# Kernel tuning notes

Hardware: AMD Instinct MI355X
Metric: run time of the kernel (lower is better)

The kernel has to match this reference:

```python
import jax, jax.numpy as jnp
import numpy as np

T, B, I, H = 512, 64, 1024, 1024
DROPOUT = 0.3


def setup_inputs() -> dict:
    key = jax.random.key(0)
    k = jax.random.split(key, 6)
    s = 1.0 / np.sqrt(H).astype(np.float32)
    x = jax.random.normal(k[0], (T, B, I), dtype=jnp.float32)
    w_ih = jax.random.uniform(k[1], (4 * H, I), minval=-s, maxval=s, dtype=jnp.float32)
    w_hh = jax.random.uniform(k[2], (4 * H, H), minval=-s, maxval=s, dtype=jnp.float32)
    b_ih = jax.random.uniform(k[3], (4 * H,), minval=-s, maxval=s, dtype=jnp.float32)
    b_hh = jax.random.uniform(k[4], (4 * H,), minval=-s, maxval=s, dtype=jnp.float32)
    # init_weights: forget-gate bias (second quarter) set to 1
    b_ih = b_ih.at[H:2 * H].set(1.0)
    b_hh = b_hh.at[H:2 * H].set(1.0)
    # DropConnect mask on recurrent weights (training-mode dropout, fixed realization)
    keep = jax.random.bernoulli(k[5], 1.0 - DROPOUT, (4 * H, H))
    hh_mask = keep.astype(jnp.float32) / (1.0 - DROPOUT)
    return {"x": x, "w_ih": w_ih, "w_hh": w_hh, "b_ih": b_ih, "b_hh": b_hh, "hh_mask": hh_mask}


def reference(x, w_ih, w_hh, b_ih, b_hh, hh_mask):
    # x: (T, B, I). PyTorch LSTM gate order: i, f, g, o.
    h = w_hh.shape[1]
    w_hh_dropped = w_hh * hh_mask  # DropConnect applied once per forward
    # Precompute input contribution for all timesteps (one big GEMM): (T, B, 4H)
    gx = jnp.einsum('tbi,gi->tbg', x, w_ih) + b_ih + b_hh

    def step(carry, g_t):
        h_t, c_t = carry
        gates = g_t + h_t @ w_hh_dropped.T  # (B, 4H)
        i_g, f_g, g_g, o_g = jnp.split(gates, 4, axis=-1)
        i_g = jax.nn.sigmoid(i_g)
        f_g = jax.nn.sigmoid(f_g)
        g_g = jnp.tanh(g_g)
        o_g = jax.nn.sigmoid(o_g)
        c_new = f_g * c_t + i_g * g_g
        h_new = o_g * jnp.tanh(c_new)
        return (h_new, c_new), h_new

    bsz = x.shape[1]
    init = (jnp.zeros((bsz, h), x.dtype), jnp.zeros((bsz, h), x.dtype))
    (hn, cn), out = jax.lax.scan(step, init, gx)
    # match torch: output (T,B,H), hn/cn with leading num_layers dim
    return out, hn[None], cn[None]
```

## Files before the change

kernel.cpp:

```cpp
#include <hip/hip_runtime.h>

#define TT 512
#define BB 64
#define II 1024
#define HH 1024
#define GG 4096
#define BH 65536
#define NBLK 128

typedef __attribute__((ext_vector_type(8))) short bf16x8;
typedef __attribute__((ext_vector_type(4))) float f32x4;
typedef __attribute__((ext_vector_type(4))) unsigned u32x4;

__device__ __forceinline__ float bf2f(unsigned short u) {
  union { unsigned int i; float f; } v; v.i = ((unsigned int)u) << 16; return v.f;
}
__device__ __forceinline__ unsigned short f2bf(float f) {
  union { float f; unsigned int i; } v; v.f = f;
  return (unsigned short)((v.i + 0x7FFFu + ((v.i >> 16) & 1u)) >> 16);
}
__device__ __forceinline__ bf16x8 pack8(float4 a, float4 b) {
  union { bf16x8 v; unsigned short u[8]; } p;
  p.u[0] = f2bf(a.x); p.u[1] = f2bf(a.y); p.u[2] = f2bf(a.z); p.u[3] = f2bf(a.w);
  p.u[4] = f2bf(b.x); p.u[5] = f2bf(b.y); p.u[6] = f2bf(b.z); p.u[7] = f2bf(b.w);
  return p.v;
}
__device__ __forceinline__ float sigmoid_f(float x) { return 1.0f / (1.0f + __expf(-x)); }
__device__ __forceinline__ float tanh_f(float x) {
  float e = __expf(-2.0f * fabsf(x));
  float t = (1.0f - e) / (1.0f + e);
  return copysignf(t, x);
}

__device__ __forceinline__ void st32_uc(unsigned* p, unsigned v) {
  __hip_atomic_store(p, v, __ATOMIC_RELAXED, __HIP_MEMORY_SCOPE_AGENT);
}
__device__ __forceinline__ unsigned ld32_uc(const unsigned* p) {
  return __hip_atomic_load(p, __ATOMIC_RELAXED, __HIP_MEMORY_SCOPE_AGENT);
}
__device__ __forceinline__ void st128_uc(void* p, u32x4 v) {
  asm volatile("global_store_dwordx4 %0, %1, off sc0 sc1" :: "v"(p), "v"(v) : "memory");
}

__global__ __launch_bounds__(256) void wdlstm_gemm_gx(
    const float* __restrict__ xc, const float* __restrict__ w_ih,
    const float* __restrict__ b_ih, const float* __restrict__ b_hh,
    unsigned short* __restrict__ gxc) {
  __shared__ __align__(16) char As[16384];
  __shared__ __align__(16) char Bs[16384];

  const int tid = threadIdx.x;
  const int bx  = blockIdx.x;
  const int tm  = bx >> 5, tn = bx & 31;
  const int m0  = tm * 128, n0 = tn * 128;
  const int wv  = tid >> 6, l = tid & 63;
  const int wr  = wv >> 1, wc = wv & 1;
  const int ln  = l & 15, lq = l >> 4;

  f32x4 acc[4][4];
#pragma unroll
  for (int i = 0; i < 4; ++i)
#pragma unroll
    for (int j = 0; j < 4; ++j) acc[i][j] = (f32x4){0.f, 0.f, 0.f, 0.f};

  for (int kt = 0; kt < 16; ++kt) {
    const int k0 = kt * 64;
    __syncthreads();
#pragma unroll
    for (int o = 0; o < 4; ++o) {
      int c2 = tid + 256 * o;
      int row = c2 >> 3, q8 = c2 & 7;
      int addr = (row * 128 + q8 * 16) ^ ((row & 7) << 4);
      {
        const float* s = xc + (size_t)(m0 + row) * II + k0 + q8 * 8;
        float4 a0 = *(const float4*)s;
        float4 a1 = *(const float4*)(s + 4);
        *(bf16x8*)(As + addr) = pack8(a0, a1);
      }
      {
        const float* s = w_ih + (size_t)(n0 + row) * II + k0 + q8 * 8;
        float4 a0 = *(const float4*)s;
        float4 a1 = *(const float4*)(s + 4);
        *(bf16x8*)(Bs + addr) = pack8(a0, a1);
      }
    }
    __syncthreads();
#pragma unroll
    for (int kc = 0; kc < 2; ++kc) {
      bf16x8 af[4], bfr[4];
#pragma unroll
      for (int mi = 0; mi < 4; ++mi) {
        int row = 64 * wr + 16 * mi + ln;
        int addr = (row * 128 + kc * 64 + lq * 16) ^ ((row & 7) << 4);
        af[mi] = *(const bf16x8*)(As + addr);
      }
#pragma unroll
      for (int ni = 0; ni < 4; ++ni) {
        int row = 64 * wc + 16 * ni + ln;
        int addr = (row * 128 + kc * 64 + lq * 16) ^ ((row & 7) << 4);
        bfr[ni] = *(const bf16x8*)(Bs + addr);
      }
#pragma unroll
      for (int mi = 0; mi < 4; ++mi)
#pragma unroll
        for (int ni = 0; ni < 4; ++ni)
          acc[mi][ni] = __builtin_amdgcn_mfma_f32_16x16x32_bf16(af[mi], bfr[ni], acc[mi][ni], 0, 0, 0);
    }
  }
#pragma unroll
  for (int mi = 0; mi < 4; ++mi)
#pragma unroll
    for (int ni = 0; ni < 4; ++ni) {
      int col = n0 + 64 * wc + 16 * ni + ln;
      float bv = b_ih[col] + b_hh[col];
#pragma unroll
      for (int r = 0; r < 4; ++r) {
        int row = m0 + 64 * wr + 16 * mi + 4 * lq + r;
        gxc[(size_t)row * GG + col] = f2bf(acc[mi][ni][r] + bv);
      }
    }
}

__global__ __launch_bounds__(256) void wdlstm_recurrence(
    const float* __restrict__ w_hh, const float* __restrict__ hh_mask,
    const unsigned short* __restrict__ gxc,
    float* __restrict__ out, float* __restrict__ c_state,
    unsigned* __restrict__ flags,
    unsigned short* __restrict__ hinit,
    unsigned short* __restrict__ hring,
    int t0, int tc) {
  __shared__ __align__(16) char Wlds[65536];
  __shared__ float Dlds[64][35];
  __shared__ __align__(16) unsigned Hs[64][4];

  const int tid = threadIdx.x;
  const int wv  = tid >> 6, l = tid & 63;
  const int ln  = l & 15, lq = l >> 4;
  const int j0h = blockIdx.x * 8;
  unsigned* g_step = flags + 2048;

#pragma unroll
  for (int c8 = 0; c8 < 16; ++c8) {
    int c = tid + 256 * c8;
    int n = c >> 7, cc = c & 127;
    int wrow = (n >> 3) * HH + j0h + (n & 7);
    const float* sw = w_hh   + (size_t)wrow * HH + cc * 8;
    const float* sm = hh_mask + (size_t)wrow * HH + cc * 8;
    float4 w0 = *(const float4*)sw, w1 = *(const float4*)(sw + 4);
    float4 m0 = *(const float4*)sm, m1 = *(const float4*)(sm + 4);
    float4 p0 = {w0.x * m0.x, w0.y * m0.y, w0.z * m0.z, w0.w * m0.w};
    float4 p1 = {w1.x * m1.x, w1.y * m1.y, w1.z * m1.z, w1.w * m1.w};
    int addr = (n * 2048 + cc * 16) ^ ((n & 7) << 4);
    *(bf16x8*)(Wlds + addr) = pack8(p0, p1);
  }
  __syncthreads();

  const int b_ep = l;
  const int jj0  = 2 * wv;
  float c_reg[2];
  if (t0 == 0) {
    c_reg[0] = c_reg[1] = 0.f;
  } else {
    float2 cv = *(const float2*)(c_state + (size_t)b_ep * HH + j0h + jj0);
    c_reg[0] = cv.x; c_reg[1] = cv.y;
  }

  float* hn_out = out + (size_t)TT * BH;
  float* cn_out = hn_out + BH;

  float gxv[4][2];
#pragma unroll
  for (int g = 0; g < 4; ++g) {
    unsigned u = *(const unsigned*)(gxc + (size_t)b_ep * GG + g * HH + j0h + jj0);
    gxv[g][0] = bf2f((unsigned short)u);
    gxv[g][1] = bf2f((unsigned short)(u >> 16));
  }

  for (int lt = 0; lt < tc; ++lt) {
    const int t = t0 + lt;

    f32x4 acc[2];
    acc[0] = (f32x4){0.f, 0.f, 0.f, 0.f};
    acc[1] = (f32x4){0.f, 0.f, 0.f, 0.f};

    if (t > 0) {
      if (blockIdx.x == 0) {
        if (tid < 64) {
          const unsigned* f0 = flags + (2 * tid) * 16;
          const unsigned* f1 = flags + (2 * tid + 1) * 16;
          while ((int)ld32_uc(f0) < t || (int)ld32_uc(f1) < t)
            __builtin_amdgcn_s_sleep(1);
          if (tid == 0) st32_uc(g_step, (unsigned)t);
        }
        __syncthreads();
      } else {
        if (tid == 0) {
          while ((int)ld32_uc(g_step) < t) __builtin_amdgcn_s_sleep(1);
        }
        __syncthreads();
      }

      const unsigned short* hp = (lt == 0) ? hinit
                                           : hring + (size_t)(lt - 1) * BH;
      const unsigned short* ap = hp + (size_t)(16 * wv + ln) * HH + lq * 8;
#pragma unroll 4
      for (int kc = 0; kc < 32; ++kc) {
        bf16x8 a = *(const bf16x8*)(ap + kc * 32);
#pragma unroll
        for (int ni = 0; ni < 2; ++ni) {
          int n = 16 * ni + ln;
          int baddr = (n * 2048 + kc * 64 + lq * 16) ^ ((n & 7) << 4);
          bf16x8 b = *(const bf16x8*)(Wlds + baddr);
          acc[ni] = __builtin_amdgcn_mfma_f32_16x16x32_bf16(a, b, acc[ni], 0, 0, 0);
        }
      }
    }
#pragma unroll
    for (int ni = 0; ni < 2; ++ni)
#pragma unroll
      for (int r = 0; r < 4; ++r)
        Dlds[16 * wv + 4 * lq + r][16 * ni + ln] = acc[ni][r];
    __syncthreads();

    float hq[2];
#pragma unroll
    for (int q = 0; q < 2; ++q) {
      float g0 = Dlds[b_ep][ 0 + jj0 + q] + gxv[0][q];
      float g1 = Dlds[b_ep][ 8 + jj0 + q] + gxv[1][q];
      float g2 = Dlds[b_ep][16 + jj0 + q] + gxv[2][q];
      float g3 = Dlds[b_ep][24 + jj0 + q] + gxv[3][q];
      float ig = sigmoid_f(g0);
      float fg = sigmoid_f(g1);
      float gg = tanh_f(g2);
      float og = sigmoid_f(g3);
      c_reg[q] = fg * c_reg[q] + ig * gg;
      hq[q] = og * tanh_f(c_reg[q]);
    }
    *(float2*)(out + (size_t)t * BH + (size_t)b_ep * HH + j0h + jj0) = make_float2(hq[0], hq[1]);
    Hs[b_ep][wv] = (unsigned)f2bf(hq[0]) | ((unsigned)f2bf(hq[1]) << 16);
    if (t == TT - 1) {
      *(float2*)(hn_out + (size_t)b_ep * HH + j0h + jj0) = make_float2(hq[0], hq[1]);
      *(float2*)(cn_out + (size_t)b_ep * HH + j0h + jj0) = make_float2(c_reg[0], c_reg[1]);
    }

    if (lt + 1 < tc) {
#pragma unroll
      for (int g = 0; g < 4; ++g) {
        unsigned u = *(const unsigned*)(gxc + ((size_t)(lt + 1) * BB + b_ep) * GG + g * HH + j0h + jj0);
        gxv[g][0] = bf2f((unsigned short)u);
        gxv[g][1] = bf2f((unsigned short)(u >> 16));
      }
    }

    __syncthreads();

    if (wv == 0) {
      u32x4 hv4 = *(const u32x4*)&Hs[l][0];
      char* dst = (char*)hring + ((size_t)lt * BH + (size_t)l * HH + j0h) * 2;
      st128_uc(dst, hv4);
      if (lt == tc - 1) {
        char* dsti = (char*)hinit + ((size_t)l * HH + j0h) * 2;
        st128_uc(dsti, hv4);
      }
      asm volatile("s_waitcnt vmcnt(0)" ::: "memory");
      if (tid == 0) st32_uc(&flags[blockIdx.x * 16], (unsigned)(t + 1));
    }
  }

  *(float2*)(c_state + (size_t)b_ep * HH + j0h + jj0) = make_float2(c_reg[0], c_reg[1]);
}

extern "C" void kernel_launch(void* const* d_in, const int* in_sizes, int n_in,
                              void* d_out, int out_size, void* d_ws, size_t ws_size,
                              hipStream_t stream) {
  const float* x       = (const float*)d_in[0];
  const float* w_ih    = (const float*)d_in[1];
  const float* w_hh    = (const float*)d_in[2];
  const float* b_ih    = (const float*)d_in[3];
  const float* b_hh    = (const float*)d_in[4];
  const float* hh_mask = (const float*)d_in[5];
  float* out           = (float*)d_out;

  char* ws = (char*)d_ws;
  float* c_state        = (float*)ws;
  unsigned* flags       = (unsigned*)(ws + 262144);
  unsigned short* hinit = (unsigned short*)(ws + 278528);
  unsigned short* hring = (unsigned short*)(ws + 409600);

  const long long fixed = 409600;
  const long long per_t = 524288 + 131072;
  long long avail = (long long)ws_size - fixed;
  int TC = (int)(avail / per_t);
  if (TC > 128) TC = 128;
  TC &= ~1;
  if (TC < 2) TC = 2;
  unsigned short* gxc = (unsigned short*)(ws + 409600 + (size_t)TC * 131072);

  hipMemsetAsync(flags, 0, 16384, stream);

  for (int t0 = 0; t0 < TT; t0 += TC) {
    int tc = TT - t0 < TC ? TT - t0 : TC;
    const float* xc = x + (size_t)t0 * BB * II;
    int grid = (tc * 64 / 128) * 32;
    wdlstm_gemm_gx<<<grid, 256, 0, stream>>>(xc, w_ih, b_ih, b_hh, gxc);
    wdlstm_recurrence<<<NBLK, 256, 0, stream>>>(w_hh, hh_mask, gxc, out, c_state,
                                                flags, hinit, hring, t0, tc);
  }
}
```

Before: 4.539 ms.

## Fuse input projection GEMM into persistent recurrence kernel with LDS-resident W_ih slice

Removes the separate big input-projection GEMM and the bf16 gate buffer. Each persistent block now keeps its slice of W_ih in LDS next to W_hh and computes the next timestep's x·W_ih product after publishing h, so that work can fill the wait before the next grid barrier. A small kernel converts x to bf16 beforehand. This doubles LDS use per block to about 128KB and puts 128 blocks' worth of input GEMM onto the serial recurrence path, so it pays off only if that work actually hides behind the barrier latency.

Result: slower. 4.663 ms (+2.7%).

```diff
diff --git a/kernel.cpp b/kernel.cpp
--- a/kernel.cpp
+++ b/kernel.cpp
@@ -42,94 +42,28 @@
   asm volatile("global_store_dwordx4 %0, %1, off sc0 sc1" :: "v"(p), "v"(v) : "memory");
 }
 
-__global__ __launch_bounds__(256) void wdlstm_gemm_gx(
-    const float* __restrict__ xc, const float* __restrict__ w_ih,
+__global__ __launch_bounds__(256) void wdlstm_xconv(
+    const float* __restrict__ xc, unsigned short* __restrict__ xbf, int n4) {
+  int stride = gridDim.x * blockDim.x;
+  for (int i = blockIdx.x * blockDim.x + threadIdx.x; i < n4; i += stride) {
+    float4 v = *(const float4*)(xc + (size_t)i * 4);
+    unsigned short o[4] = {f2bf(v.x), f2bf(v.y), f2bf(v.z), f2bf(v.w)};
+    *(unsigned long long*)(xbf + (size_t)i * 4) = *(unsigned long long*)o;
+  }
+}
+
+__global__ __launch_bounds__(256) void wdlstm_fused(
+    const float* __restrict__ w_hh, const float* __restrict__ hh_mask,
+    const float* __restrict__ w_ih,
     const float* __restrict__ b_ih, const float* __restrict__ b_hh,
-    unsigned short* __restrict__ gxc) {
-  __shared__ __align__(16) char As[16384];
-  __shared__ __align__(16) char Bs[16384];
-
-  const int tid = threadIdx.x;
-  const int bx  = blockIdx.x;
-  const int tm  = bx >> 5, tn = bx & 31;
-  const int m0  = tm * 128, n0 = tn * 128;
-  const int wv  = tid >> 6, l = tid & 63;
-  const int wr  = wv >> 1, wc = wv & 1;
-  const int ln  = l & 15, lq = l >> 4;
-
-  f32x4 acc[4][4];
-#pragma unroll
-  for (int i = 0; i < 4; ++i)
-#pragma unroll
-    for (int j = 0; j < 4; ++j) acc[i][j] = (f32x4){0.f, 0.f, 0.f, 0.f};
-
-  for (int kt = 0; kt < 16; ++kt) {
-    const int k0 = kt * 64;
-    __syncthreads();
-#pragma unroll
-    for (int o = 0; o < 4; ++o) {
-      int c2 = tid + 256 * o;
-      int row = c2 >> 3, q8 = c2 & 7;
-      int addr = (row * 128 + q8 * 16) ^ ((row & 7) << 4);
-      {
-        const float* s = xc + (size_t)(m0 + row) * II + k0 + q8 * 8;
-        float4 a0 = *(const float4*)s;
-        float4 a1 = *(const float4*)(s + 4);
-        *(bf16x8*)(As + addr) = pack8(a0, a1);
-      }
-      {
-        const float* s = w_ih + (size_t)(n0 + row) * II + k0 + q8 * 8;
-        float4 a0 = *(const float4*)s;
-        float4 a1 = *(const float4*)(s + 4);
-        *(bf16x8*)(Bs + addr) = pack8(a0, a1);
-      }
-    }
-    __syncthreads();
-#pragma unroll
-    for (int kc = 0; kc < 2; ++kc) {
-      bf16x8 af[4], bfr[4];
-#pragma unroll
-      for (int mi = 0; mi < 4; ++mi) {
-        int row = 64 * wr + 16 * mi + ln;
-        int addr = (row * 128 + kc * 64 + lq * 16) ^ ((row & 7) << 4);
-        af[mi] = *(const bf16x8*)(As + addr);
-      }
-#pragma unroll
-      for (int ni = 0; ni < 4; ++ni) {
-        int row = 64 * wc + 16 * ni + ln;
-        int addr = (row * 128 + kc * 64 + lq * 16) ^ ((row & 7) << 4);
-        bfr[ni] = *(const bf16x8*)(Bs + addr);
-      }
-#pragma unroll
-      for (int mi = 0; mi < 4; ++mi)
-#pragma unroll
-        for (int ni = 0; ni < 4; ++ni)
-          acc[mi][ni] = __builtin_amdgcn_mfma_f32_16x16x32_bf16(af[mi], bfr[ni], acc[mi][ni], 0, 0, 0);
-    }
-  }
-#pragma unroll
-  for (int mi = 0; mi < 4; ++mi)
-#pragma unroll
-    for (int ni = 0; ni < 4; ++ni) {
-      int col = n0 + 64 * wc + 16 * ni + ln;
-      float bv = b_ih[col] + b_hh[col];
-#pragma unroll
-      for (int r = 0; r < 4; ++r) {
-        int row = m0 + 64 * wr + 16 * mi + 4 * lq + r;
-        gxc[(size_t)row * GG + col] = f2bf(acc[mi][ni][r] + bv);
-      }
-    }
-}
-
-__global__ __launch_bounds__(256) void wdlstm_recurrence(
-    const float* __restrict__ w_hh, const float* __restrict__ hh_mask,
-    const unsigned short* __restrict__ gxc,
+    const unsigned short* __restrict__ xbf,
     float* __restrict__ out, float* __restrict__ c_state,
     unsigned* __restrict__ flags,
     unsigned short* __restrict__ hinit,
     unsigned short* __restrict__ hring,
     int t0, int tc) {
-  __shared__ __align__(16) char Wlds[65536];
+  __shared__ __align__(16) char Wh[65536];
+  __shared__ __align__(16) char Wi[65536];
   __shared__ float Dlds[64][35];
   __shared__ __align__(16) unsigned Hs[64][4];
 
@@ -144,14 +78,21 @@
     int c = tid + 256 * c8;
     int n = c >> 7, cc = c & 127;
     int wrow = (n >> 3) * HH + j0h + (n & 7);
-    const float* sw = w_hh   + (size_t)wrow * HH + cc * 8;
-    const float* sm = hh_mask + (size_t)wrow * HH + cc * 8;
-    float4 w0 = *(const float4*)sw, w1 = *(const float4*)(sw + 4);
-    float4 m0 = *(const float4*)sm, m1 = *(const float4*)(sm + 4);
-    float4 p0 = {w0.x * m0.x, w0.y * m0.y, w0.z * m0.z, w0.w * m0.w};
-    float4 p1 = {w1.x * m1.x, w1.y * m1.y, w1.z * m1.z, w1.w * m1.w};
     int addr = (n * 2048 + cc * 16) ^ ((n & 7) << 4);
-    *(bf16x8*)(Wlds + addr) = pack8(p0, p1);
+    {
+      const float* sw = w_hh   + (size_t)wrow * HH + cc * 8;
+      const float* sm = hh_mask + (size_t)wrow * HH + cc * 8;
+      float4 w0 = *(const float4*)sw, w1 = *(const float4*)(sw + 4);
+      float4 m0 = *(const float4*)sm, m1 = *(const float4*)(sm + 4);
+      float4 p0 = {w0.x * m0.x, w0.y * m0.y, w0.z * m0.z, w0.w * m0.w};
+      float4 p1 = {w1.x * m1.x, w1.y * m1.y, w1.z * m1.z, w1.w * m1.w};
+      *(bf16x8*)(Wh + addr) = pack8(p0, p1);
+    }
+    {
+      const float* si = w_ih + (size_t)wrow * II + cc * 8;
+      float4 a0 = *(const float4*)si, a1 = *(const float4*)(si + 4);
+      *(bf16x8*)(Wi + addr) = pack8(a0, a1);
+    }
   }
   __syncthreads();
 
@@ -164,24 +105,41 @@
     float2 cv = *(const float2*)(c_state + (size_t)b_ep * HH + j0h + jj0);
     c_reg[0] = cv.x; c_reg[1] = cv.y;
   }
+  float biasv[4][2];
+#pragma unroll
+  for (int g = 0; g < 4; ++g)
+#pragma unroll
+    for (int q = 0; q < 2; ++q) {
+      int col = g * HH + j0h + jj0 + q;
+      biasv[g][q] = b_ih[col] + b_hh[col];
+    }
 
   float* hn_out = out + (size_t)TT * BH;
   float* cn_out = hn_out + BH;
 
-  float gxv[4][2];
-#pragma unroll
-  for (int g = 0; g < 4; ++g) {
-    unsigned u = *(const unsigned*)(gxc + (size_t)b_ep * GG + g * HH + j0h + jj0);
-    gxv[g][0] = bf2f((unsigned short)u);
-    gxv[g][1] = bf2f((unsigned short)(u >> 16));
-  }
+  f32x4 gxacc[2];
+  auto gx_compute = [&](int lt) {
+    gxacc[0] = (f32x4){0.f, 0.f, 0.f, 0.f};
+    gxacc[1] = (f32x4){0.f, 0.f, 0.f, 0.f};
+    const unsigned short* ap = xbf + (size_t)lt * BH + (size_t)(16 * wv + ln) * II + lq * 8;
+#pragma unroll 4
+    for (int kc = 0; kc < 32; ++kc) {
+      bf16x8 a = *(const bf16x8*)(ap + kc * 32);
+#pragma unroll
+      for (int ni = 0; ni < 2; ++ni) {
+        int n = 16 * ni + ln;
+        int baddr = (n * 2048 + kc * 64 + lq * 16) ^ ((n & 7) << 4);
+        bf16x8 b = *(const bf16x8*)(Wi + baddr);
+        gxacc[ni] = __builtin_amdgcn_mfma_f32_16x16x32_bf16(a, b, gxacc[ni], 0, 0, 0);
+      }
+    }
+  };
+  gx_compute(0);
 
   for (int lt = 0; lt < tc; ++lt) {
     const int t = t0 + lt;
 
-    f32x4 acc[2];
-    acc[0] = (f32x4){0.f, 0.f, 0.f, 0.f};
-    acc[1] = (f32x4){0.f, 0.f, 0.f, 0.f};
+    f32x4 acc[2] = {gxacc[0], gxacc[1]};
 
     if (t > 0) {
       if (blockIdx.x == 0) {
@@ -210,7 +168,7 @@
         for (int ni = 0; ni < 2; ++ni) {
           int n = 16 * ni + ln;
           int baddr = (n * 2048 + kc * 64 + lq * 16) ^ ((n & 7) << 4);
-          bf16x8 b = *(const bf16x8*)(Wlds + baddr);
+          bf16x8 b = *(const bf16x8*)(Wh + baddr);
           acc[ni] = __builtin_amdgcn_mfma_f32_16x16x32_bf16(a, b, acc[ni], 0, 0, 0);
         }
       }
@@ -225,10 +183,10 @@
     float hq[2];
 #pragma unroll
     for (int q = 0; q < 2; ++q) {
-      float g0 = Dlds[b_ep][ 0 + jj0 + q] + gxv[0][q];
-      float g1 = Dlds[b_ep][ 8 + jj0 + q] + gxv[1][q];
-      float g2 = Dlds[b_ep][16 + jj0 + q] + gxv[2][q];
-      float g3 = Dlds[b_ep][24 + jj0 + q] + gxv[3][q];
+      float g0 = Dlds[b_ep][ 0 + jj0 + q] + biasv[0][q];
+      float g1 = Dlds[b_ep][ 8 + jj0 + q] + biasv[1][q];
+      float g2 = Dlds[b_ep][16 + jj0 + q] + biasv[2][q];
+      float g3 = Dlds[b_ep][24 + jj0 + q] + biasv[3][q];
       float ig = sigmoid_f(g0);
       float fg = sigmoid_f(g1);
       float gg = tanh_f(g2);
@@ -241,15 +199,6 @@
     if (t == TT - 1) {
       *(float2*)(hn_out + (size_t)b_ep * HH + j0h + jj0) = make_float2(hq[0], hq[1]);
       *(float2*)(cn_out + (size_t)b_ep * HH + j0h + jj0) = make_float2(c_reg[0], c_reg[1]);
-    }
-
-    if (lt + 1 < tc) {
-#pragma unroll
-      for (int g = 0; g < 4; ++g) {
-        unsigned u = *(const unsigned*)(gxc + ((size_t)(lt + 1) * BB + b_ep) * GG + g * HH + j0h + jj0);
-        gxv[g][0] = bf2f((unsigned short)u);
-        gxv[g][1] = bf2f((unsigned short)(u >> 16));
-      }
     }
 
     __syncthreads();
@@ -265,6 +214,8 @@
       asm volatile("s_waitcnt vmcnt(0)" ::: "memory");
       if (tid == 0) st32_uc(&flags[blockIdx.x * 16], (unsigned)(t + 1));
     }
+
+    if (lt + 1 < tc) gx_compute(lt + 1);
   }
 
   *(float2*)(c_state + (size_t)b_ep * HH + j0h + jj0) = make_float2(c_reg[0], c_reg[1]);
@@ -288,22 +239,20 @@
   unsigned short* hring = (unsigned short*)(ws + 409600);
 
   const long long fixed = 409600;
-  const long long per_t = 524288 + 131072;
+  const long long per_t = 131072 + 131072;
   long long avail = (long long)ws_size - fixed;
   int TC = (int)(avail / per_t);
   if (TC > 128) TC = 128;
-  TC &= ~1;
   if (TC < 2) TC = 2;
-  unsigned short* gxc = (unsigned short*)(ws + 409600 + (size_t)TC * 131072);
+  unsigned short* xbf = (unsigned short*)(ws + 409600 + (size_t)TC * 131072);
 
   hipMemsetAsync(flags, 0, 16384, stream);
 
   for (int t0 = 0; t0 < TT; t0 += TC) {
     int tc = TT - t0 < TC ? TT - t0 : TC;
     const float* xc = x + (size_t)t0 * BB * II;
-    int grid = (tc * 64 / 128) * 32;
-    wdlstm_gemm_gx<<<grid, 256, 0, stream>>>(xc, w_ih, b_ih, b_hh, gxc);
-    wdlstm_recurrence<<<NBLK, 256, 0, stream>>>(w_hh, hh_mask, gxc, out, c_state,
-                                                flags, hinit, hring, t0, tc);
-  }
-}
+    wdlstm_xconv<<<256, 256, 0, stream>>>(xc, xbf, tc * BH / 4);
+    wdlstm_fused<<<NBLK, 256, 0, stream>>>(w_hh, hh_mask, w_ih, b_ih, b_hh, xbf,
+                                           out, c_state, flags, hinit, hring, t0, tc);
+  }
+}
```
